# Kernel tuning notes

Measured on AMD Instinct MI355X. Metric: run time of the kernel, lower is better.

## Reference

```python
import jax, jax.numpy as jnp
import numpy as np

B, N, D, C = 8, 400, 768, 3
K = 0.4
# Original keeps ranked positions whose argsort value (original index) < k*N.
# That count is static: M = #{j in [0,N) : j < k*N}
M = int(np.sum(np.arange(N) < K * N))  # 160
# static off-diagonal pair index lists (i != j), row-major like the nested loops
_ii, _jj = np.nonzero(~np.eye(M, dtype=bool))
II = jnp.asarray(_ii)
JJ = jnp.asarray(_jj)


def setup_inputs() -> dict:
    key = jax.random.key(0)
    k1, k2, k3, k4 = jax.random.split(key, 4)
    x = jax.random.normal(k1, (B, N, D), dtype=jnp.float32)
    w_span = jax.random.normal(k2, (D, 1), dtype=jnp.float32) * 0.02
    b_span = jnp.zeros((1,), dtype=jnp.float32)
    w_pair = jax.random.normal(k3, (3 * D, C), dtype=jnp.float32) * 0.02
    b_pair = jnp.zeros((C,), dtype=jnp.float32)
    span_ranges = jax.random.randint(k4, (N, 2), 0, 40, dtype=jnp.int32)
    return {"x": x, "w_span": w_span, "b_span": b_span,
            "w_pair": w_pair, "b_pair": b_pair, "span_ranges": span_ranges}


def reference(x, w_span, b_span, w_pair, b_pair, span_ranges):
    # span scorer: Linear(D,1) + sigmoid -> [B, N]
    h = jax.nn.sigmoid(x @ w_span + b_span)[..., 0]
    # torch.argsort(descending=True)
    order = jnp.argsort(-h, axis=-1)  # [B, N], original span indices in rank order
    # keep ranked positions j where order[b, j] < k*N (exactly M per row)
    pos = jnp.sort(jnp.where(order < K * N, jnp.arange(N), N), axis=-1)[:, :M]  # [B, M]
    # gather selected spans (built under no_grad in the original)
    x_ranked = jax.lax.stop_gradient(jnp.take_along_axis(x, pos[:, :, None], axis=1))  # [B, M, D]
    ranges_ranked = span_ranges[pos]  # [B, M, 2]

    # pair scorer decomposed over the concat [x_i, x_j, x_i*x_j]
    w1, w2, w3 = w_pair[:D], w_pair[D:2 * D], w_pair[2 * D:]
    a = x_ranked @ w1  # [B, M, C] contribution of x_i
    b = x_ranked @ w2  # [B, M, C] contribution of x_j
    mult = x_ranked[:, :, None, :] * x_ranked[:, None, :, :]  # [B, M, M, D]
    logits = a[:, :, None, :] + b[:, None, :, :] + mult @ w3 + b_pair  # [B, M, M, C]
    probs = jax.nn.softmax(jax.nn.sigmoid(logits), axis=-1)

    pair_probs = probs[:, II, JJ]  # [B, M*(M-1), C], off-diagonal pairs
    pair_ranges = jnp.stack([ranges_ranked[:, II], ranges_ranked[:, JJ]], axis=2)  # [B, P, 2, 2]
    return pair_probs, pair_ranges
```

## Files before the change

### kernel.cpp

```cpp
#include <hip/hip_runtime.h>
#include <math.h>

constexpr int B_ = 8;
constexpr int N_ = 400;
constexpr int D_ = 768;
constexpr int M_ = 160;
constexpr int PAIRS_ = M_ * (M_ - 1);
constexpr size_t BND_ = (size_t)B_ * N_ * D_;

typedef __attribute__((ext_vector_type(8))) short short8;
typedef __attribute__((ext_vector_type(4))) float floatx4;


__device__ __forceinline__ short f2bf(float f) {
  unsigned u = __float_as_uint(f);
  return (short)((u + 0x7fffu + ((u >> 16) & 1u)) >> 16);
}

__global__ __launch_bounds__(256) void k_prep(const float* __restrict__ x,
                                              const float* __restrict__ w_span,
                                              const float* __restrict__ w_pair,
                                              const float* __restrict__ b_pair,
                                              double* __restrict__ z,
                                              float* __restrict__ aterm,
                                              float* __restrict__ bterm,
                                              short* __restrict__ Xbf,
                                              short* __restrict__ Ybf) {
  int row = blockIdx.x * 4 + (threadIdx.x >> 6);
  int lane = threadIdx.x & 63;
  const float* xr = x + (size_t)row * D_;
  const float* w3 = w_pair + 2 * D_ * 3;

  double acc = 0.0;
  float a0 = 0, a1 = 0, a2 = 0, c0 = 0, c1 = 0, c2 = 0;
#pragma unroll
  for (int it = 0; it < 3; ++it) {
    int d = it * 256 + lane * 4;
    float4 xv = *(const float4*)(xr + d);
    float4 sv = *(const float4*)(w_span + d);
    acc += (double)xv.x * sv.x + (double)xv.y * sv.y +
           (double)xv.z * sv.z + (double)xv.w * sv.w;
    float xf[4] = {xv.x, xv.y, xv.z, xv.w};

    float w1v[12], w2v[12], w3v[12];
#pragma unroll
    for (int q = 0; q < 3; ++q) {
      *(float4*)(w1v + 4 * q) = *(const float4*)(w_pair + (size_t)d * 3 + 4 * q);
      *(float4*)(w2v + 4 * q) = *(const float4*)(w_pair + (size_t)(D_ + d) * 3 + 4 * q);
      *(float4*)(w3v + 4 * q) = *(const float4*)(w3 + (size_t)d * 3 + 4 * q);
    }
#pragma unroll
    for (int e = 0; e < 4; ++e) {
      a0 += xf[e] * w1v[e * 3 + 0];
      a1 += xf[e] * w1v[e * 3 + 1];
      a2 += xf[e] * w1v[e * 3 + 2];
      c0 += xf[e] * w2v[e * 3 + 0];
      c1 += xf[e] * w2v[e * 3 + 1];
      c2 += xf[e] * w2v[e * 3 + 2];
    }

    size_t o = (size_t)row * D_ + d;
    *(short4*)(Xbf + o) = make_short4(f2bf(xf[0]), f2bf(xf[1]), f2bf(xf[2]), f2bf(xf[3]));
#pragma unroll
    for (int c = 0; c < 3; ++c) {
      *(short4*)(Ybf + (size_t)c * BND_ + o) =
          make_short4(f2bf(xf[0] * w3v[0 * 3 + c]), f2bf(xf[1] * w3v[1 * 3 + c]),
                      f2bf(xf[2] * w3v[2 * 3 + c]), f2bf(xf[3] * w3v[3 * 3 + c]));
    }
  }
#pragma unroll
  for (int off = 32; off > 0; off >>= 1) {
    acc += __shfl_down(acc, off, 64);
    a0 += __shfl_down(a0, off, 64);
    a1 += __shfl_down(a1, off, 64);
    a2 += __shfl_down(a2, off, 64);
    c0 += __shfl_down(c0, off, 64);
    c1 += __shfl_down(c1, off, 64);
    c2 += __shfl_down(c2, off, 64);
  }
  if (lane == 0) {
    z[row] = acc;
    aterm[row * 3 + 0] = a0 + b_pair[0];
    aterm[row * 3 + 1] = a1 + b_pair[1];
    aterm[row * 3 + 2] = a2 + b_pair[2];
    bterm[row * 3 + 0] = c0;
    bterm[row * 3 + 1] = c1;
    bterm[row * 3 + 2] = c2;
  }
}

__global__ __launch_bounds__(256) void k_rank(const double* __restrict__ z,
                                              int* __restrict__ pos) {
  __shared__ double zsh[N_];
  __shared__ int ranksh[M_];
  int b = blockIdx.x;
  int t = threadIdx.x;
  for (int j = t; j < N_; j += 256) zsh[j] = z[b * N_ + j];
  __syncthreads();
  if (t < M_) {
    double zi = zsh[t];
    int cnt = 0;
    for (int j = 0; j < N_; ++j) {
      double zj = zsh[j];
      cnt += (zj > zi) || (zj == zi && j < t);
    }
    ranksh[t] = cnt;
  }
  __syncthreads();
  if (t < M_) {
    int r = ranksh[t];
    int slot = 0;
#pragma unroll 8
    for (int k = 0; k < M_; ++k) slot += (ranksh[k] < r);
    pos[b * M_ + slot] = r;
  }
}

__global__ __launch_bounds__(256) void k_pairs(const short* __restrict__ Xbf,
                                               const short* __restrict__ Ybf,
                                               const int* __restrict__ pos,
                                               const float* __restrict__ aterm,
                                               const float* __restrict__ bterm,
                                               const int* __restrict__ span_ranges,
                                               float* __restrict__ out_probs,
                                               float4* __restrict__ out_ranges) {
  __shared__ float red[3 * 64 * 13];

  int lane = threadIdx.x & 63;
  int wv = threadIdx.x >> 6;
  int blk = blockIdx.x;
  int b = blk / 100;
  int t = blk - b * 100;
  int ti = t / 10;
  int tj = t - ti * 10;
  int quad = lane >> 4;
  int l16 = lane & 15;

  const int* posb = pos + b * M_;
  int pa = posb[ti * 16 + l16];
  int pb = posb[tj * 16 + l16];
  size_t oa = ((size_t)(b * N_ + pa)) * D_ + wv * 192 + quad * 8;
  size_t ob = ((size_t)(b * N_ + pb)) * D_ + wv * 192 + quad * 8;

  const short* ah0 = Ybf + 0 * BND_ + oa;
  const short* ah1 = Ybf + 1 * BND_ + oa;
  const short* ah2 = Ybf + 2 * BND_ + oa;
  const short* bhp = Xbf + ob;

  floatx4 acc0 = {0.f, 0.f, 0.f, 0.f};
  floatx4 acc1 = {0.f, 0.f, 0.f, 0.f};
  floatx4 acc2 = {0.f, 0.f, 0.f, 0.f};

#pragma unroll
  for (int k = 0; k < 192; k += 32) {
    short8 bh = *(const short8*)(bhp + k);
    short8 h0 = *(const short8*)(ah0 + k);
    short8 h1 = *(const short8*)(ah1 + k);
    short8 h2 = *(const short8*)(ah2 + k);
    acc0 = __builtin_amdgcn_mfma_f32_16x16x32_bf16(h0, bh, acc0, 0, 0, 0);
    acc1 = __builtin_amdgcn_mfma_f32_16x16x32_bf16(h1, bh, acc1, 0, 0, 0);
    acc2 = __builtin_amdgcn_mfma_f32_16x16x32_bf16(h2, bh, acc2, 0, 0, 0);
  }

  if (wv > 0) {
    int base = ((wv - 1) * 64 + lane) * 13;
#pragma unroll
    for (int r = 0; r < 4; ++r) {
      red[base + r] = acc0[r];
      red[base + 4 + r] = acc1[r];
      red[base + 8 + r] = acc2[r];
    }
  }
  __syncthreads();
  if (wv != 0) return;

#pragma unroll
  for (int u = 0; u < 3; ++u) {
    int base = (u * 64 + lane) * 13;
#pragma unroll
    for (int r = 0; r < 4; ++r) {
      acc0[r] += red[base + r];
      acc1[r] += red[base + 4 + r];
      acc2[r] += red[base + 8 + r];
    }
  }

  const float* at = aterm + (size_t)(b * N_) * 3;
  const float* bt = bterm + (size_t)(b * N_) * 3;
  int j = tj * 16 + l16;
  float bj0 = bt[pb * 3 + 0], bj1 = bt[pb * 3 + 1], bj2 = bt[pb * 3 + 2];
  int rj0 = span_ranges[pb * 2 + 0], rj1 = span_ranges[pb * 2 + 1];

#pragma unroll
  for (int r = 0; r < 4; ++r) {
    int i = ti * 16 + quad * 4 + r;
    if (i == j) continue;
    int pi = posb[i];
    float l0 = acc0[r] + at[pi * 3 + 0] + bj0;
    float l1 = acc1[r] + at[pi * 3 + 1] + bj1;
    float l2 = acc2[r] + at[pi * 3 + 2] + bj2;
    float s0 = 1.0f / (1.0f + expf(-l0));
    float s1 = 1.0f / (1.0f + expf(-l1));
    float s2 = 1.0f / (1.0f + expf(-l2));
    float e0 = expf(s0), e1 = expf(s1), e2 = expf(s2);
    float inv = 1.0f / (e0 + e1 + e2);
    int jj = j - (j > i ? 1 : 0);
    size_t p = (size_t)b * PAIRS_ + (size_t)i * (M_ - 1) + jj;
    out_probs[p * 3 + 0] = e0 * inv;
    out_probs[p * 3 + 1] = e1 * inv;
    out_probs[p * 3 + 2] = e2 * inv;
    float4 rg;
    rg.x = (float)span_ranges[pi * 2 + 0];
    rg.y = (float)span_ranges[pi * 2 + 1];
    rg.z = (float)rj0;
    rg.w = (float)rj1;
    out_ranges[p] = rg;
  }
}

extern "C" void kernel_launch(void* const* d_in, const int* in_sizes, int n_in,
                              void* d_out, int out_size, void* d_ws, size_t ws_size,
                              hipStream_t stream) {
  const float* x = (const float*)d_in[0];
  const float* w_span = (const float*)d_in[1];
  const float* w_pair = (const float*)d_in[3];
  const float* b_pair = (const float*)d_in[4];
  const int* span_ranges = (const int*)d_in[5];

  char* ws = (char*)d_ws;
  double* z = (double*)ws;
  int* pos = (int*)(ws + 25600);
  float* aterm = (float*)(ws + 30720);
  float* bterm = (float*)(ws + 69120);
  short* Xbf = (short*)(ws + 107520);
  short* Ybf = (short*)(ws + 5022720);

  float* out = (float*)d_out;
  float* out_probs = out;
  float4* out_ranges = (float4*)(out + (size_t)B_ * PAIRS_ * 3);

  k_prep<<<(B_ * N_) / 4, 256, 0, stream>>>(x, w_span, w_pair, b_pair, z,
                                            aterm, bterm, Xbf, Ybf);
  k_rank<<<B_, 256, 0, stream>>>(z, pos);
  k_pairs<<<B_ * 100, 256, 0, stream>>>(Xbf, Ybf, pos, aterm, bterm,
                                        span_ranges, out_probs, out_ranges);
}
```

Baseline: 107.4 us.

## Fuse bf16 conversion and w3 scaling into pair kernel, drop prep bf16 buffers

The prep kernel no longer writes bf16 copies of x and the three w3-scaled copies. The pair kernel instead reads fp32 x and w3 directly, converts to bf16 by truncation, and scales by w3 in registers before the MFMAs. This removes about 25 MB of workspace writes and their later reads. In exchange, the pair kernel reads fp32 rows (twice the bytes per element) and repeats the conversion work across tiles. Rounding changes from round-to-nearest to truncation.

Measured after the change: 106.4 us (median of 2 runs). Within noise of the previous version (-0.9%).

```diff
diff --git a/kernel.cpp b/kernel.cpp
--- a/kernel.cpp
+++ b/kernel.cpp
@@ -6,30 +6,21 @@
 constexpr int D_ = 768;
 constexpr int M_ = 160;
 constexpr int PAIRS_ = M_ * (M_ - 1);
-constexpr size_t BND_ = (size_t)B_ * N_ * D_;
 
 typedef __attribute__((ext_vector_type(8))) short short8;
 typedef __attribute__((ext_vector_type(4))) float floatx4;
 
 
-__device__ __forceinline__ short f2bf(float f) {
-  unsigned u = __float_as_uint(f);
-  return (short)((u + 0x7fffu + ((u >> 16) & 1u)) >> 16);
-}
-
-__global__ __launch_bounds__(256) void k_prep(const float* __restrict__ x,
-                                              const float* __restrict__ w_span,
-                                              const float* __restrict__ w_pair,
-                                              const float* __restrict__ b_pair,
-                                              double* __restrict__ z,
-                                              float* __restrict__ aterm,
-                                              float* __restrict__ bterm,
-                                              short* __restrict__ Xbf,
-                                              short* __restrict__ Ybf) {
+__global__ __launch_bounds__(256) void k_span_ab(const float* __restrict__ x,
+                                                 const float* __restrict__ w_span,
+                                                 const float* __restrict__ w_pair,
+                                                 const float* __restrict__ b_pair,
+                                                 double* __restrict__ z,
+                                                 float* __restrict__ aterm,
+                                                 float* __restrict__ bterm) {
   int row = blockIdx.x * 4 + (threadIdx.x >> 6);
   int lane = threadIdx.x & 63;
   const float* xr = x + (size_t)row * D_;
-  const float* w3 = w_pair + 2 * D_ * 3;
 
   double acc = 0.0;
   float a0 = 0, a1 = 0, a2 = 0, c0 = 0, c1 = 0, c2 = 0;
@@ -42,12 +33,11 @@
            (double)xv.z * sv.z + (double)xv.w * sv.w;
     float xf[4] = {xv.x, xv.y, xv.z, xv.w};
 
-    float w1v[12], w2v[12], w3v[12];
+    float w1v[12], w2v[12];
 #pragma unroll
     for (int q = 0; q < 3; ++q) {
       *(float4*)(w1v + 4 * q) = *(const float4*)(w_pair + (size_t)d * 3 + 4 * q);
       *(float4*)(w2v + 4 * q) = *(const float4*)(w_pair + (size_t)(D_ + d) * 3 + 4 * q);
-      *(float4*)(w3v + 4 * q) = *(const float4*)(w3 + (size_t)d * 3 + 4 * q);
     }
 #pragma unroll
     for (int e = 0; e < 4; ++e) {
@@ -57,15 +47,6 @@
       c0 += xf[e] * w2v[e * 3 + 0];
       c1 += xf[e] * w2v[e * 3 + 1];
       c2 += xf[e] * w2v[e * 3 + 2];
-    }
-
-    size_t o = (size_t)row * D_ + d;
-    *(short4*)(Xbf + o) = make_short4(f2bf(xf[0]), f2bf(xf[1]), f2bf(xf[2]), f2bf(xf[3]));
-#pragma unroll
-    for (int c = 0; c < 3; ++c) {
-      *(short4*)(Ybf + (size_t)c * BND_ + o) =
-          make_short4(f2bf(xf[0] * w3v[0 * 3 + c]), f2bf(xf[1] * w3v[1 * 3 + c]),
-                      f2bf(xf[2] * w3v[2 * 3 + c]), f2bf(xf[3] * w3v[3 * 3 + c]));
     }
   }
 #pragma unroll
@@ -116,8 +97,8 @@
   }
 }
 
-__global__ __launch_bounds__(256) void k_pairs(const short* __restrict__ Xbf,
-                                               const short* __restrict__ Ybf,
+__global__ __launch_bounds__(256) void k_pairs(const float* __restrict__ x,
+                                               const float* __restrict__ w_pair,
                                                const int* __restrict__ pos,
                                                const float* __restrict__ aterm,
                                                const float* __restrict__ bterm,
@@ -139,13 +120,9 @@
   const int* posb = pos + b * M_;
   int pa = posb[ti * 16 + l16];
   int pb = posb[tj * 16 + l16];
-  size_t oa = ((size_t)(b * N_ + pa)) * D_ + wv * 192 + quad * 8;
-  size_t ob = ((size_t)(b * N_ + pb)) * D_ + wv * 192 + quad * 8;
-
-  const short* ah0 = Ybf + 0 * BND_ + oa;
-  const short* ah1 = Ybf + 1 * BND_ + oa;
-  const short* ah2 = Ybf + 2 * BND_ + oa;
-  const short* bhp = Xbf + ob;
+  const float* xa = x + ((size_t)(b * N_ + pa)) * D_ + wv * 192 + quad * 8;
+  const float* xb = x + ((size_t)(b * N_ + pb)) * D_ + wv * 192 + quad * 8;
+  const float* w3 = w_pair + 2 * D_ * 3;
 
   floatx4 acc0 = {0.f, 0.f, 0.f, 0.f};
   floatx4 acc1 = {0.f, 0.f, 0.f, 0.f};
@@ -153,13 +130,29 @@
 
 #pragma unroll
   for (int k = 0; k < 192; k += 32) {
-    short8 bh = *(const short8*)(bhp + k);
-    short8 h0 = *(const short8*)(ah0 + k);
-    short8 h1 = *(const short8*)(ah1 + k);
-    short8 h2 = *(const short8*)(ah2 + k);
-    acc0 = __builtin_amdgcn_mfma_f32_16x16x32_bf16(h0, bh, acc0, 0, 0, 0);
-    acc1 = __builtin_amdgcn_mfma_f32_16x16x32_bf16(h1, bh, acc1, 0, 0, 0);
-    acc2 = __builtin_amdgcn_mfma_f32_16x16x32_bf16(h2, bh, acc2, 0, 0, 0);
+    float af[8], bfv[8], wv24[24];
+    *(float4*)(af + 0) = *(const float4*)(xa + k + 0);
+    *(float4*)(af + 4) = *(const float4*)(xa + k + 4);
+    *(float4*)(bfv + 0) = *(const float4*)(xb + k + 0);
+    *(float4*)(bfv + 4) = *(const float4*)(xb + k + 4);
+    const float* wp = w3 + (size_t)(wv * 192 + k + quad * 8) * 3;
+#pragma unroll
+    for (int q = 0; q < 6; ++q) *(float4*)(wv24 + 4 * q) = *(const float4*)(wp + 4 * q);
+
+    short8 bh;
+#pragma unroll
+    for (int e = 0; e < 8; ++e) bh[e] = (short)(__float_as_uint(bfv[e]) >> 16);
+
+#pragma unroll
+    for (int c = 0; c < 3; ++c) {
+      short8 h;
+#pragma unroll
+      for (int e = 0; e < 8; ++e)
+        h[e] = (short)(__float_as_uint(af[e] * wv24[e * 3 + c]) >> 16);
+      floatx4 acc = (c == 0) ? acc0 : (c == 1) ? acc1 : acc2;
+      acc = __builtin_amdgcn_mfma_f32_16x16x32_bf16(h, bh, acc, 0, 0, 0);
+      if (c == 0) acc0 = acc; else if (c == 1) acc1 = acc; else acc2 = acc;
+    }
   }
 
   if (wv > 0) {
@@ -232,16 +225,14 @@
   int* pos = (int*)(ws + 25600);
   float* aterm = (float*)(ws + 30720);
   float* bterm = (float*)(ws + 69120);
-  short* Xbf = (short*)(ws + 107520);
-  short* Ybf = (short*)(ws + 5022720);
 
   float* out = (float*)d_out;
   float* out_probs = out;
   float4* out_ranges = (float4*)(out + (size_t)B_ * PAIRS_ * 3);
 
-  k_prep<<<(B_ * N_) / 4, 256, 0, stream>>>(x, w_span, w_pair, b_pair, z,
-                                            aterm, bterm, Xbf, Ybf);
+  k_span_ab<<<(B_ * N_) / 4, 256, 0, stream>>>(x, w_span, w_pair, b_pair, z,
+                                               aterm, bterm);
   k_rank<<<B_, 256, 0, stream>>>(z, pos);
-  k_pairs<<<B_ * 100, 256, 0, stream>>>(Xbf, Ybf, pos, aterm, bterm,
+  k_pairs<<<B_ * 100, 256, 0, stream>>>(x, w_pair, pos, aterm, bterm,
                                         span_ranges, out_probs, out_ranges);
 }
```
